# Kernel tuning notes

Measured on AMD Instinct MI355X. Metric: run time of the kernel, lower is better.

## Reference

```python
import jax, jax.numpy as jnp
import numpy as np

COS_EPS = 1e-8  # torch F.cosine_similarity eps


def setup_inputs() -> dict:
    key = jax.random.key(0)
    k1, k2 = jax.random.split(key)
    x = jax.random.normal(k1, (8192, 512), dtype=jnp.float32)
    class_logits = jax.random.normal(k2, (8192, 100), dtype=jnp.float32)
    return {"x": x, "class_logits": class_logits}


def reference(x, class_logits):
    N, D = x.shape
    C = class_logits.shape[1]

    # class_logits.clone().detach()
    logits = jax.lax.stop_gradient(class_logits)
    pred = jax.nn.softmax(logits, axis=1)
    max_logit = pred.max(axis=1)          # [N]
    max_cls = pred.argmax(axis=1)         # [N] int

    # graph(): pairwise cosine similarity = normalize rows + gram matmul
    norms = jnp.linalg.norm(x, axis=1, keepdims=True)
    xn = x / jnp.maximum(norms, COS_EPS)
    mat = xn @ xn.T                       # [N, N]

    x_agg = mat @ x + x                   # [N, D]
    x_new = jax.lax.stop_gradient(x_agg)

    # update_prototype: per-class weighted scatter-add then mean over counts
    weighted = x_new * max_logit[:, None]                     # [N, D]
    sums = jax.ops.segment_sum(weighted, max_cls, num_segments=C)      # [C, D]
    counts = jax.ops.segment_sum(jnp.ones((N,), x.dtype), max_cls, num_segments=C)  # [C]
    prototypes = jnp.where(counts[:, None] > 0,
                           sums / jnp.maximum(counts, 1.0)[:, None],
                           jnp.zeros_like(sums))              # [C, D]

    # inter_class_matrix[i, j] = prototypes[j] - prototypes[i]
    inter_class_matrix = prototypes[None, :, :] - prototypes[:, None, :]  # [C, C, D]
    return prototypes, inter_class_matrix
```

## Files before the change

### kernel.cpp

```cpp
#include <hip/hip_runtime.h>
#include <math.h>

#define N_ROWS 8192
#define D_DIM  512
#define C_CLS  100

typedef unsigned short u16;
typedef unsigned int u32;
typedef __attribute__((ext_vector_type(8))) _Float16 half8;
typedef __attribute__((ext_vector_type(4))) float floatx4;

#define WS_G      0
#define WS_GP     262144
#define WS_INV    5505024
#define WS_WV     5513216
#define WS_CLS    5521408
#define WS_CNT    5529600
#define WS_OFFS   5529728
#define WS_ORDER  5529856
#define WS_U      5538048
#define WS_V      5589248
#define WS_ZTH    5640448

#define LDA 517

typedef const __attribute__((address_space(1))) u32* gp32;
typedef __attribute__((address_space(3))) u32* lp32;
__device__ __forceinline__ void cp16(const u16* g, u16* l) {
    __builtin_amdgcn_global_load_lds((gp32)g, (lp32)l, 16, 0, 0);
}

__device__ __forceinline__ u16 f2h(float v) {
    _Float16 h = (_Float16)v;
    return *(u16*)&h;
}

__global__ __launch_bounds__(256) void kA(const float* __restrict__ logits,
        const float* __restrict__ x, float* __restrict__ wv, int* __restrict__ cls,
        float* __restrict__ inv, u16* __restrict__ zth) {
    __shared__ float xs[16 * LDA];
    __shared__ float ns[4][16];
    __shared__ float sv_s[16];
    int bx = blockIdx.x, t = threadIdx.x;
    if (bx < 1024) {
        int lane = t & 63;
        int row0 = (bx << 3) + ((t >> 6) << 1);
        #pragma unroll
        for (int rr = 0; rr < 2; ++rr) {
            int row = row0 + rr;
            const float* lrow = logits + (size_t)row * C_CLS;
            float v1 = lrow[lane];
            bool has2 = (lane + 64) < C_CLS;
            float v2 = has2 ? lrow[lane + 64] : -INFINITY;
            float m; int idx;
            if (v2 > v1) { m = v2; idx = lane + 64; } else { m = v1; idx = lane; }
            #pragma unroll
            for (int off = 32; off >= 1; off >>= 1) {
                float om = __shfl_down(m, off);
                int   oi = __shfl_down(idx, off);
                if (om > m || (om == m && oi < idx)) { m = om; idx = oi; }
            }
            m = __shfl(m, 0);
            idx = __shfl(idx, 0);
            float s = expf(v1 - m) + (has2 ? expf(v2 - m) : 0.0f);
            #pragma unroll
            for (int off = 32; off >= 1; off >>= 1) s += __shfl_down(s, off);
            if (lane == 0) {
                wv[row] = 1.0f / s;
                cls[row] = idx;
            }
        }
        return;
    }
    int r0 = (bx - 1024) << 4;
    const float* src = x + (size_t)r0 * D_DIM;
    #pragma unroll
    for (int i = 0; i < 8; ++i) {
        int e = i * 1024 + t * 4;
        int r = e >> 9, c = e & 511;
        *(float4*)&xs[r * LDA + c] = *(const float4*)&src[e];
    }
    __syncthreads();
    {
        int r = t & 15, seg = t >> 4;
        const float* row = &xs[r * LDA + seg * 32];
        float ss = 0.f;
        #pragma unroll
        for (int jj = 0; jj < 32; ++jj) { float v = row[jj]; ss += v * v; }
        ns[0][r] = 0.f;
        __syncthreads();
        atomicAdd(&ns[0][r], ss);
    }
    __syncthreads();
    if (t < 16) {
        float iv = 1.0f / fmaxf(sqrtf(ns[0][t]), 1e-8f);
        inv[r0 + t] = iv;
        sv_s[t] = sqrtf(iv);
    }
    __syncthreads();
    int c = t >> 1, rq = (t & 1) * 8;
    float svl[8];
    #pragma unroll
    for (int ii = 0; ii < 8; ++ii) svl[ii] = sv_s[rq + ii];
    #pragma unroll
    for (int ct = 0; ct < 4; ++ct) {
        int d = ct * 128 + c;
        u16 o[8];
        #pragma unroll
        for (int ii = 0; ii < 8; ++ii)
            o[ii] = f2h(xs[(rq + ii) * LDA + d] * svl[ii]);
        uint4 val = make_uint4((u32)o[0] | ((u32)o[1] << 16),
                               (u32)o[2] | ((u32)o[3] << 16),
                               (u32)o[4] | ((u32)o[5] << 16),
                               (u32)o[6] | ((u32)o[7] << 16));
        *(uint4*)&zth[(size_t)d * N_ROWS + r0 + rq] = val;
    }
}

__global__ __launch_bounds__(1024) void kB(const int* __restrict__ cls,
        int* __restrict__ cnt, int* __restrict__ offs, int* __restrict__ order) {
    __shared__ int hist[128], scan_s[128], cur[128];
    int t = threadIdx.x;
    if (t < 128) hist[t] = 0;
    __syncthreads();
    for (int m = t; m < N_ROWS; m += 1024) atomicAdd(&hist[cls[m]], 1);
    __syncthreads();
    if (t < 128) scan_s[t] = hist[t];
    __syncthreads();
    #pragma unroll
    for (int d = 1; d < 128; d <<= 1) {
        int add = (t < 128 && t >= d) ? scan_s[t - d] : 0;
        __syncthreads();
        if (t < 128) scan_s[t] += add;
        __syncthreads();
    }
    if (t < 128) {
        int off0 = scan_s[t] - hist[t];
        cur[t] = off0;
        offs[t] = off0;
        cnt[t] = hist[t];
    }
    __syncthreads();
    for (int m = t; m < N_ROWS; m += 1024) {
        int p = atomicAdd(&cur[cls[m]], 1);
        order[p] = m;
    }
}

__global__ __launch_bounds__(256) void kC(const u16* __restrict__ zth,
        const float* __restrict__ x, const float* __restrict__ inv,
        const float* __restrict__ wv, const int* __restrict__ order,
        const int* __restrict__ offs, const int* __restrict__ cnt,
        float* __restrict__ Gp, float* __restrict__ u_arr, float* __restrict__ v_arr) {
    __shared__ __attribute__((aligned(16))) union {
        struct { u16 Ah[2][128 * 32], Bh[2][128 * 32]; } g;
        struct { float us[4][64], vs[4][64]; } uv;
    } sm;
    int bx = blockIdx.x, t = threadIdx.x;
    if (bx >= 320) {
        int idx = bx - 320;
        int c = idx >> 3, jc = idx & 7;
        int g = t >> 6, lane = t & 63;
        int j = jc * 64 + lane;
        int n = cnt[c], o = offs[c];
        float ua = 0.f, va = 0.f;
        for (int p = g; p < n; p += 4) {
            int m = order[o + p];
            float wm = wv[m];
            float wi = wm * inv[m];
            float xv = x[(size_t)m * D_DIM + j];
            ua += wi * xv; va += wm * xv;
        }
        sm.uv.us[g][lane] = ua; sm.uv.vs[g][lane] = va;
        __syncthreads();
        if (g == 0) {
            u_arr[(size_t)c * D_DIM + j] = sm.uv.us[0][lane] + sm.uv.us[1][lane] + sm.uv.us[2][lane] + sm.uv.us[3][lane];
            v_arr[(size_t)c * D_DIM + j] = sm.uv.vs[0][lane] + sm.uv.vs[1][lane] + sm.uv.vs[2][lane] + sm.uv.vs[3][lane];
        }
        return;
    }
    int tile = bx % 10;
    int p = bx / 10;
    int ti = tile < 4 ? 0 : (tile < 7 ? 1 : (tile < 9 ? 2 : 3));
    int tj = tile - (ti == 0 ? 0 : (ti == 1 ? 3 : (ti == 2 ? 5 : 6)));
    int i0 = ti << 7, j0 = tj << 7;
    bool diag = (ti == tj);
    int kb = p << 8;
    int w = t >> 6, l = t & 63;
    int srow = t >> 2, scol = (t & 3) << 3;
    int lm = l & 15, lg = l >> 4;
    floatx4 acc[4][4];
    #pragma unroll
    for (int mi = 0; mi < 4; ++mi)
        #pragma unroll
        for (int ni = 0; ni < 4; ++ni) acc[mi][ni] = (floatx4){0.f, 0.f, 0.f, 0.f};
    int d0 = srow * 32 + scol;
    int d1 = (64 + srow) * 32 + scol;
    const size_t ga0 = (size_t)(i0 + srow) * N_ROWS + kb + scol;
    const size_t ga1 = (size_t)(i0 + 64 + srow) * N_ROWS + kb + scol;
    const size_t gb0 = (size_t)(j0 + srow) * N_ROWS + kb + scol;
    const size_t gb1 = (size_t)(j0 + 64 + srow) * N_ROWS + kb + scol;
    cp16(zth + ga0, sm.g.Ah[0] + d0);
    cp16(zth + ga1, sm.g.Ah[0] + d1);
    if (!diag) {
        cp16(zth + gb0, sm.g.Bh[0] + d0);
        cp16(zth + gb1, sm.g.Bh[0] + d1);
    }
    __syncthreads();
    for (int s = 0; s < 8; ++s) {
        int cur = s & 1, nxt = cur ^ 1;
        if (s + 1 < 8) {
            int ks = (s + 1) << 5;
            cp16(zth + ga0 + ks, sm.g.Ah[nxt] + d0);
            cp16(zth + ga1 + ks, sm.g.Ah[nxt] + d1);
            if (!diag) {
                cp16(zth + gb0 + ks, sm.g.Bh[nxt] + d0);
                cp16(zth + gb1 + ks, sm.g.Bh[nxt] + d1);
            }
        }
        const u16* Bhs = diag ? sm.g.Ah[cur] : sm.g.Bh[cur];
        half8 ah[4], bh[4];
        #pragma unroll
        for (int mi = 0; mi < 4; ++mi) {
            int off = (((w & 1) << 6) + (mi << 4) + lm) * 32 + (lg << 3);
            ah[mi] = *(const half8*)&sm.g.Ah[cur][off];
        }
        #pragma unroll
        for (int ni = 0; ni < 4; ++ni) {
            int off = (((w >> 1) << 6) + (ni << 4) + lm) * 32 + (lg << 3);
            bh[ni] = *(const half8*)&Bhs[off];
        }
        #pragma unroll
        for (int mi = 0; mi < 4; ++mi)
            #pragma unroll
            for (int ni = 0; ni < 4; ++ni)
                acc[mi][ni] = __builtin_amdgcn_mfma_f32_16x16x32_f16(ah[mi], bh[ni], acc[mi][ni], 0, 0, 0);
        __syncthreads();
    }
    float* Gb = Gp + ((size_t)(p * 10 + tile) << 14);
    #pragma unroll
    for (int mi = 0; mi < 4; ++mi) {
        int row0 = ((w & 1) << 6) + (mi << 4) + (lg << 2);
        #pragma unroll
        for (int ni = 0; ni < 4; ++ni) {
            int col = ((w >> 1) << 6) + (ni << 4) + lm;
            #pragma unroll
            for (int r = 0; r < 4; ++r)
                Gb[(size_t)(row0 + r) * 128 + col] = acc[mi][ni][r];
        }
    }
}

__global__ __launch_bounds__(256) void kR(const float* __restrict__ Gp,
                                          float* __restrict__ G) {
    int i = blockIdx.x * 256 + threadIdx.x;
    int r = i >> 9, c = i & 511;
    int tr = r >> 7, tc = c >> 7, rr = r & 127, cc = c & 127;
    if (tr > tc) { int tmp = tr; tr = tc; tc = tmp; tmp = rr; rr = cc; cc = tmp; }
    int tid = tr * 4 + tc - ((tr * (tr + 1)) >> 1);
    const float* src = Gp + ((size_t)tid << 14) + rr * 128 + cc;
    float s = 0.f;
    #pragma unroll
    for (int p = 0; p < 32; ++p) s += src[(size_t)p * 163840];
    G[i] = s;
}

__global__ __launch_bounds__(256) void kD(const float* __restrict__ u_arr,
        const float* __restrict__ v_arr, const int* __restrict__ cnt,
        const float* __restrict__ G, float* __restrict__ out) {
    __shared__ float us[8][512];
    int g = blockIdx.x >> 4;
    int panel = blockIdx.x & 15;
    int t = threadIdx.x;
    for (int idx = t; idx < 8 * 512; idx += 256) {
        int ci = idx >> 9, k = idx & 511;
        int cc = g * 8 + ci;
        us[ci][k] = (cc < C_CLS) ? u_arr[(size_t)cc * D_DIM + k] : 0.f;
    }
    __syncthreads();
    int ci = t >> 5, cj = t & 31;
    int c = g * 8 + ci;
    int j = panel * 32 + cj;
    float acc = 0.f;
    #pragma unroll 8
    for (int k = 0; k < D_DIM; ++k)
        acc += us[ci][k] * G[(size_t)k * D_DIM + j];
    if (c < C_CLS) {
        int n = cnt[c];
        float s = (n > 0) ? 1.0f / (float)n : 0.0f;
        out[(size_t)c * D_DIM + j] = (v_arr[(size_t)c * D_DIM + j] + acc) * s;
    }
}

__global__ __launch_bounds__(256) void kE(const float* __restrict__ proto,
                                          float* __restrict__ inter) {
    int pair = blockIdx.x * 4 + (threadIdx.x >> 6);
    int i = pair / C_CLS;
    int j = pair - i * C_CLS;
    int d = (threadIdx.x & 63) << 3;
    float4 pj0 = *(const float4*)&proto[j * D_DIM + d];
    float4 pj1 = *(const float4*)&proto[j * D_DIM + d + 4];
    float4 pi0 = *(const float4*)&proto[i * D_DIM + d];
    float4 pi1 = *(const float4*)&proto[i * D_DIM + d + 4];
    float4 r0, r1;
    r0.x = pj0.x - pi0.x; r0.y = pj0.y - pi0.y; r0.z = pj0.z - pi0.z; r0.w = pj0.w - pi0.w;
    r1.x = pj1.x - pi1.x; r1.y = pj1.y - pi1.y; r1.z = pj1.z - pi1.z; r1.w = pj1.w - pi1.w;
    *(float4*)&inter[(size_t)pair * D_DIM + d]     = r0;
    *(float4*)&inter[(size_t)pair * D_DIM + d + 4] = r1;
}

extern "C" void kernel_launch(void* const* d_in, const int* in_sizes, int n_in,
                              void* d_out, int out_size, void* d_ws, size_t ws_size,
                              hipStream_t stream) {
    const float* x      = (const float*)d_in[0];
    const float* logits = (const float*)d_in[1];
    float* out = (float*)d_out;
    float* ws  = (float*)d_ws;
    float* G     = ws + WS_G;
    float* Gp    = ws + WS_GP;
    float* inv   = ws + WS_INV;
    float* wv    = ws + WS_WV;
    int*   cls   = (int*)(ws + WS_CLS);
    int*   cnt   = (int*)(ws + WS_CNT);
    int*   offs  = (int*)(ws + WS_OFFS);
    int*   order = (int*)(ws + WS_ORDER);
    float* u_arr = ws + WS_U;
    float* v_arr = ws + WS_V;
    u16* zth = (u16*)(ws + WS_ZTH);

    kA<<<1536, 256, 0, stream>>>(logits, x, wv, cls, inv, zth);
    kB<<<1, 1024, 0, stream>>>(cls, cnt, offs, order);
    kC<<<1120, 256, 0, stream>>>(zth, x, inv, wv, order, offs, cnt, Gp, u_arr, v_arr);
    kR<<<1024, 256, 0, stream>>>(Gp, G);
    kD<<<208, 256, 0, stream>>>(u_arr, v_arr, cnt, G, out);
    kE<<<C_CLS * C_CLS / 4, 256, 0, stream>>>(out, out + C_CLS * D_DIM);
}
```

Before: 168.1 us.

## Drop class-sort kernel, ballot-scan classes, lengthen Gram K-split with swizzled LDS

Removes the single-block histogram/scan/order kernel. Class counts now come from atomics in the softmax kernel, and the per-class u/v accumulation scans the class array with wavefront ballots instead of using a sorted index list. The Gram kernel's K-split is reduced from 32 to 8 partitions, each looping 32 steps, which cuts the partial-sum buffer and the reduction work. An XOR swizzle on LDS slots is added to avoid bank conflicts. The trade-offs are fewer Gram blocks, which lowers parallelism, and the ballot scan now reading all 8192 class labels per class block.

```diff
diff --git a/kernel.cpp b/kernel.cpp
--- a/kernel.cpp
+++ b/kernel.cpp
@@ -16,8 +16,6 @@
 #define WS_WV     5513216
 #define WS_CLS    5521408
 #define WS_CNT    5529600
-#define WS_OFFS   5529728
-#define WS_ORDER  5529856
 #define WS_U      5538048
 #define WS_V      5589248
 #define WS_ZTH    5640448
@@ -37,7 +35,7 @@
 
 __global__ __launch_bounds__(256) void kA(const float* __restrict__ logits,
         const float* __restrict__ x, float* __restrict__ wv, int* __restrict__ cls,
-        float* __restrict__ inv, u16* __restrict__ zth) {
+        float* __restrict__ inv, u16* __restrict__ zth, int* __restrict__ cnt) {
     __shared__ float xs[16 * LDA];
     __shared__ float ns[4][16];
     __shared__ float sv_s[16];
@@ -68,6 +66,7 @@
             if (lane == 0) {
                 wv[row] = 1.0f / s;
                 cls[row] = idx;
+                atomicAdd(&cnt[idx], 1);
             }
         }
         return;
@@ -117,59 +116,34 @@
     }
 }
 
-__global__ __launch_bounds__(1024) void kB(const int* __restrict__ cls,
-        int* __restrict__ cnt, int* __restrict__ offs, int* __restrict__ order) {
-    __shared__ int hist[128], scan_s[128], cur[128];
-    int t = threadIdx.x;
-    if (t < 128) hist[t] = 0;
-    __syncthreads();
-    for (int m = t; m < N_ROWS; m += 1024) atomicAdd(&hist[cls[m]], 1);
-    __syncthreads();
-    if (t < 128) scan_s[t] = hist[t];
-    __syncthreads();
-    #pragma unroll
-    for (int d = 1; d < 128; d <<= 1) {
-        int add = (t < 128 && t >= d) ? scan_s[t - d] : 0;
-        __syncthreads();
-        if (t < 128) scan_s[t] += add;
-        __syncthreads();
-    }
-    if (t < 128) {
-        int off0 = scan_s[t] - hist[t];
-        cur[t] = off0;
-        offs[t] = off0;
-        cnt[t] = hist[t];
-    }
-    __syncthreads();
-    for (int m = t; m < N_ROWS; m += 1024) {
-        int p = atomicAdd(&cur[cls[m]], 1);
-        order[p] = m;
-    }
-}
-
 __global__ __launch_bounds__(256) void kC(const u16* __restrict__ zth,
         const float* __restrict__ x, const float* __restrict__ inv,
-        const float* __restrict__ wv, const int* __restrict__ order,
-        const int* __restrict__ offs, const int* __restrict__ cnt,
+        const float* __restrict__ wv, const int* __restrict__ cls,
         float* __restrict__ Gp, float* __restrict__ u_arr, float* __restrict__ v_arr) {
     __shared__ __attribute__((aligned(16))) union {
         struct { u16 Ah[2][128 * 32], Bh[2][128 * 32]; } g;
         struct { float us[4][64], vs[4][64]; } uv;
     } sm;
     int bx = blockIdx.x, t = threadIdx.x;
-    if (bx >= 320) {
-        int idx = bx - 320;
+    if (bx >= 80) {
+        int idx = bx - 80;
         int c = idx >> 3, jc = idx & 7;
         int g = t >> 6, lane = t & 63;
         int j = jc * 64 + lane;
-        int n = cnt[c], o = offs[c];
         float ua = 0.f, va = 0.f;
-        for (int p = g; p < n; p += 4) {
-            int m = order[o + p];
-            float wm = wv[m];
-            float wi = wm * inv[m];
-            float xv = x[(size_t)m * D_DIM + j];
-            ua += wi * xv; va += wm * xv;
+        int base = g * 2048;
+        for (int b = 0; b < 2048; b += 64) {
+            int mb = base + b;
+            unsigned long long mask = __ballot(cls[mb + lane] == c);
+            while (mask) {
+                int bit = __builtin_ctzll(mask);
+                mask &= mask - 1;
+                int m = mb + bit;
+                float wm = wv[m];
+                float wi = wm * inv[m];
+                float xv = x[(size_t)m * D_DIM + j];
+                ua += wi * xv; va += wm * xv;
+            }
         }
         sm.uv.us[g][lane] = ua; sm.uv.vs[g][lane] = va;
         __syncthreads();
@@ -185,21 +159,23 @@
     int tj = tile - (ti == 0 ? 0 : (ti == 1 ? 3 : (ti == 2 ? 5 : 6)));
     int i0 = ti << 7, j0 = tj << 7;
     bool diag = (ti == tj);
-    int kb = p << 8;
+    int kb = p << 10;
     int w = t >> 6, l = t & 63;
-    int srow = t >> 2, scol = (t & 3) << 3;
+    int srow = t >> 2, slot = t & 3;
+    int xslot = slot ^ ((srow >> 1) & 3);
     int lm = l & 15, lg = l >> 4;
+    int rs = (lm >> 1) & 3;
     floatx4 acc[4][4];
     #pragma unroll
     for (int mi = 0; mi < 4; ++mi)
         #pragma unroll
         for (int ni = 0; ni < 4; ++ni) acc[mi][ni] = (floatx4){0.f, 0.f, 0.f, 0.f};
-    int d0 = srow * 32 + scol;
-    int d1 = (64 + srow) * 32 + scol;
-    const size_t ga0 = (size_t)(i0 + srow) * N_ROWS + kb + scol;
-    const size_t ga1 = (size_t)(i0 + 64 + srow) * N_ROWS + kb + scol;
-    const size_t gb0 = (size_t)(j0 + srow) * N_ROWS + kb + scol;
-    const size_t gb1 = (size_t)(j0 + 64 + srow) * N_ROWS + kb + scol;
+    int d0 = srow * 32 + slot * 8;
+    int d1 = (64 + srow) * 32 + slot * 8;
+    const size_t ga0 = (size_t)(i0 + srow) * N_ROWS + kb + (xslot << 3);
+    const size_t ga1 = (size_t)(i0 + 64 + srow) * N_ROWS + kb + (xslot << 3);
+    const size_t gb0 = (size_t)(j0 + srow) * N_ROWS + kb + (xslot << 3);
+    const size_t gb1 = (size_t)(j0 + 64 + srow) * N_ROWS + kb + (xslot << 3);
     cp16(zth + ga0, sm.g.Ah[0] + d0);
     cp16(zth + ga1, sm.g.Ah[0] + d1);
     if (!diag) {
@@ -207,9 +183,9 @@
         cp16(zth + gb1, sm.g.Bh[0] + d1);
     }
     __syncthreads();
-    for (int s = 0; s < 8; ++s) {
+    for (int s = 0; s < 32; ++s) {
         int cur = s & 1, nxt = cur ^ 1;
-        if (s + 1 < 8) {
+        if (s + 1 < 32) {
             int ks = (s + 1) << 5;
             cp16(zth + ga0 + ks, sm.g.Ah[nxt] + d0);
             cp16(zth + ga1 + ks, sm.g.Ah[nxt] + d1);
@@ -222,12 +198,12 @@
         half8 ah[4], bh[4];
         #pragma unroll
         for (int mi = 0; mi < 4; ++mi) {
-            int off = (((w & 1) << 6) + (mi << 4) + lm) * 32 + (lg << 3);
+            int off = (((w & 1) << 6) + (mi << 4) + lm) * 32 + ((lg ^ rs) << 3);
             ah[mi] = *(const half8*)&sm.g.Ah[cur][off];
         }
         #pragma unroll
         for (int ni = 0; ni < 4; ++ni) {
-            int off = (((w >> 1) << 6) + (ni << 4) + lm) * 32 + (lg << 3);
+            int off = (((w >> 1) << 6) + (ni << 4) + lm) * 32 + ((lg ^ rs) << 3);
             bh[ni] = *(const half8*)&Bhs[off];
         }
         #pragma unroll
@@ -261,7 +237,7 @@
     const float* src = Gp + ((size_t)tid << 14) + rr * 128 + cc;
     float s = 0.f;
     #pragma unroll
-    for (int p = 0; p < 32; ++p) s += src[(size_t)p * 163840];
+    for (int p = 0; p < 8; ++p) s += src[(size_t)p * 163840];
     G[i] = s;
 }
 
@@ -322,15 +298,13 @@
     float* wv    = ws + WS_WV;
     int*   cls   = (int*)(ws + WS_CLS);
     int*   cnt   = (int*)(ws + WS_CNT);
-    int*   offs  = (int*)(ws + WS_OFFS);
-    int*   order = (int*)(ws + WS_ORDER);
     float* u_arr = ws + WS_U;
     float* v_arr = ws + WS_V;
     u16* zth = (u16*)(ws + WS_ZTH);
 
-    kA<<<1536, 256, 0, stream>>>(logits, x, wv, cls, inv, zth);
-    kB<<<1, 1024, 0, stream>>>(cls, cnt, offs, order);
-    kC<<<1120, 256, 0, stream>>>(zth, x, inv, wv, order, offs, cnt, Gp, u_arr, v_arr);
+    hipMemsetAsync(cnt, 0, 128 * sizeof(int), stream);
+    kA<<<1536, 256, 0, stream>>>(logits, x, wv, cls, inv, zth, cnt);
+    kC<<<880, 256, 0, stream>>>(zth, x, inv, wv, cls, Gp, u_arr, v_arr);
     kR<<<1024, 256, 0, stream>>>(Gp, G);
     kD<<<208, 256, 0, stream>>>(u_arr, v_arr, cnt, G, out);
     kE<<<C_CLS * C_CLS / 4, 256, 0, stream>>>(out, out + C_CLS * D_DIM);
```

Result: no change. 170.8 us (+1.7%).
